# Kernel optimization log

Measured on AMD Instinct MI355X. Metric: run time of the kernel, lower is better.

Reference implementation:

```python
import jax, jax.numpy as jnp
import numpy as np

EPS = 1e-6

def elu_feature_map(x):
    return jax.nn.elu(x) + 1.0

def setup_inputs() -> dict:
    key = jax.random.key(0)
    kq, kk, kv = jax.random.split(key, 3)
    B, N, L, S, H, D, M = 4, 8, 1024, 1024, 8, 64, 64
    queries = jax.random.normal(kq, (B, N, L, H, D), dtype=jnp.float32)
    keys = jax.random.normal(kk, (B, N, S, H, D), dtype=jnp.float32)
    values = jax.random.normal(kv, (B, N, S, H, M), dtype=jnp.float32)
    key_mask = jnp.ones((B, S), dtype=jnp.float32)  # key_lengths.float_matrix (all valid)
    return {"queries": queries, "keys": keys, "values": values, "key_mask": key_mask}

def reference(queries, keys, values, key_mask):
    # Q: [B,N,L,H,D], K: [B,N,S,H,D], V: [B,N,S,H,M], key_mask: [B,S]
    Q = elu_feature_map(queries)
    K = elu_feature_map(keys) * key_mask[:, None, :, None, None]
    # KV state: [B,N,H,M,D]
    KV = jnp.einsum('bnshd,bnshm->bnhmd', K, values)
    # normalizer: [B,N,L,H]
    Z = 1.0 / (jnp.einsum('bnlhd,bnhd->bnlh', Q, K.sum(axis=2)) + EPS)
    # output: [B,N,L,H,M]
    V = jnp.einsum('bnlhd,bnhmd,bnlh->bnlhm', Q, KV, Z)
    return V
```

## Files before the change

kernel.cpp:

```cpp
#include <hip/hip_runtime.h>
#include <hip/hip_bf16.h>


constexpr int Bc = 4, Nc = 8, Hc = 8;
constexpr int Lc = 1024, Sc = 1024, Dc = 64, Mc = 64;
constexpr int HD = Hc * Dc;
constexpr int GROUPS = Bc * Nc * Hc;
constexpr int SPLITS = 4;
constexpr int SROWS = Sc / SPLITS;
constexpr int LSPLITS = 4;
constexpr int LROWS = Lc / LSPLITS;
constexpr int PARTIAL = Dc * Mc + Dc;
constexpr int NTS = SROWS / 32;
constexpr int NTL = LROWS / 64;
constexpr int PADS = 36;
constexpr int PADD = 68;
constexpr float EPSF = 1e-6f;

typedef __attribute__((ext_vector_type(8))) __bf16 bf16x8;
typedef __attribute__((ext_vector_type(4))) float f32x4;

__device__ __forceinline__ float elup1(float x) {
    return x > 0.0f ? x + 1.0f : __expf(x);
}
__device__ __forceinline__ unsigned short f2bf(float f) {
    unsigned u = __builtin_bit_cast(unsigned, f);
    u += 0x7fffu + ((u >> 16) & 1u);
    return (unsigned short)(u >> 16);
}
__device__ __forceinline__ unsigned packbf(float lo, float hi) {
    return (unsigned)f2bf(lo) | ((unsigned)f2bf(hi) << 16);
}

__global__ void __launch_bounds__(256, 4)
la_kv_mfma(const float* __restrict__ Kg, const float* __restrict__ Vg,
           const float* __restrict__ Mg, float* __restrict__ ws)
{
    __shared__ unsigned short kt[Dc][PADS];
    __shared__ unsigned short vt[Mc][PADS];
    __shared__ float ksred[16][64];

    const int t    = threadIdx.x;
    const int tx   = t & 15;
    const int tyq  = t >> 4;
    const int lane = t & 63;
    const int w    = t >> 6;
    const int g    = blockIdx.y;
    const int sp   = blockIdx.x;
    const int h    = g & 7;
    const int bn   = g >> 3;
    const int b    = g >> 6;

    const size_t rowbase = (size_t)bn * Sc * HD + (size_t)h * Dc;
    const size_t mbase   = (size_t)b * Sc;
    const int    sbase   = sp * SROWS;

    float4 kr0, kr1, vr0, vr1;
    float  mr0, mr1;
    float  ksp[4] = {0.f, 0.f, 0.f, 0.f};

    auto loadA = [&](int it) {
        const int s0 = sbase + it * 32 + 2 * tyq;
        const size_t off = rowbase + (size_t)s0 * HD + 4 * tx;
        kr0 = *reinterpret_cast<const float4*>(Kg + off);
        kr1 = *reinterpret_cast<const float4*>(Kg + off + HD);
        vr0 = *reinterpret_cast<const float4*>(Vg + off);
        vr1 = *reinterpret_cast<const float4*>(Vg + off + HD);
        mr0 = Mg[mbase + s0];
        mr1 = Mg[mbase + s0 + 1];
    };
    auto storeA = [&]() {
        const float k0[4] = {kr0.x, kr0.y, kr0.z, kr0.w};
        const float k1[4] = {kr1.x, kr1.y, kr1.z, kr1.w};
        const float v0[4] = {vr0.x, vr0.y, vr0.z, vr0.w};
        const float v1[4] = {vr1.x, vr1.y, vr1.z, vr1.w};
        #pragma unroll
        for (int i = 0; i < 4; ++i) {
            const float a0 = elup1(k0[i]) * mr0;
            const float a1 = elup1(k1[i]) * mr1;
            ksp[i] += a0 + a1;
            *reinterpret_cast<unsigned*>(&kt[4 * tx + i][2 * tyq]) = packbf(a0, a1);
            *reinterpret_cast<unsigned*>(&vt[4 * tx + i][2 * tyq]) = packbf(v0[i], v1[i]);
        }
    };

    f32x4 acc[4];
    #pragma unroll
    for (int ms = 0; ms < 4; ++ms) acc[ms] = (f32x4){0.f, 0.f, 0.f, 0.f};

    const int fcol = 8 * (lane >> 4);
    const int frow = lane & 15;

    loadA(0);
    storeA();
    __syncthreads();
    for (int it = 0; it < NTS; ++it) {
        if (it + 1 < NTS) loadA(it + 1);
        union { bf16x8 v; uint2 u[2]; } fa;
        {
            const uint2* p = reinterpret_cast<const uint2*>(&kt[16 * w + frow][fcol]);
            fa.u[0] = p[0]; fa.u[1] = p[1];
        }
        #pragma unroll
        for (int ms = 0; ms < 4; ++ms) {
            union { bf16x8 v; uint2 u[2]; } fb;
            const uint2* p = reinterpret_cast<const uint2*>(&vt[16 * ms + frow][fcol]);
            fb.u[0] = p[0]; fb.u[1] = p[1];
            acc[ms] = __builtin_amdgcn_mfma_f32_16x16x32_bf16(fa.v, fb.v, acc[ms], 0, 0, 0);
        }
        __syncthreads();
        if (it + 1 < NTS) storeA();
        __syncthreads();
    }

    float* outp = ws + (size_t)(g * SPLITS + sp) * PARTIAL;
    #pragma unroll
    for (int ms = 0; ms < 4; ++ms)
        #pragma unroll
        for (int r = 0; r < 4; ++r)
            outp[(16 * w + 4 * (lane >> 4) + r) * Mc + 16 * ms + frow] = acc[ms][r];

    #pragma unroll
    for (int i = 0; i < 4; ++i) ksred[tyq][4 * tx + i] = ksp[i];
    __syncthreads();
    if (t < 64) {
        float s = 0.f;
        #pragma unroll
        for (int j = 0; j < 16; ++j) s += ksred[j][t];
        outp[Dc * Mc + t] = s;
    }
}

__global__ void __launch_bounds__(256, 4)
la_out_mfma(const float* __restrict__ Qg, const float* __restrict__ ws,
            float* __restrict__ Og)
{
    __shared__ unsigned short kvm[Mc][PADD];
    __shared__ unsigned short ksb[64];
    __shared__ unsigned short qb[64][PADD];

    const int t    = threadIdx.x;
    const int tx   = t & 15;
    const int tyq  = t >> 4;
    const int lane = t & 63;
    const int w    = t >> 6;
    const int g    = blockIdx.y;
    const int ls   = blockIdx.x;
    const int h    = g & 7;
    const int bn   = g >> 3;

    const size_t rowbase = (size_t)bn * Lc * HD + (size_t)h * Dc;
    const float* pw = ws + (size_t)g * SPLITS * PARTIAL;
    const int lbase = ls * LROWS;

    float4 qr[4];
    auto loadB = [&](int it) {
        const int l0 = lbase + it * 64 + 4 * tyq;
        #pragma unroll
        for (int j = 0; j < 4; ++j)
            qr[j] = *reinterpret_cast<const float4*>(Qg + rowbase + (size_t)(l0 + j) * HD + 4 * tx);
    };
    auto storeB = [&]() {
        #pragma unroll
        for (int j = 0; j < 4; ++j) {
            const int r = 4 * tyq + j;
            const float q[4] = {qr[j].x, qr[j].y, qr[j].z, qr[j].w};
            uint2 pk;
            pk.x = packbf(elup1(q[0]), elup1(q[1]));
            pk.y = packbf(elup1(q[2]), elup1(q[3]));
            *reinterpret_cast<uint2*>(&qb[r][4 * tx]) = pk;
        }
    };

    loadB(0);
    #pragma unroll
    for (int e = 0; e < 16; ++e) {
        const int idx = t + 256 * e;
        const float s = pw[idx] + pw[PARTIAL + idx] + pw[2 * PARTIAL + idx] + pw[3 * PARTIAL + idx];
        kvm[idx & 63][idx >> 6] = f2bf(s);
    }
    if (t < 64) {
        const float s = pw[Dc * Mc + t] + pw[PARTIAL + Dc * Mc + t]
                      + pw[2 * PARTIAL + Dc * Mc + t] + pw[3 * PARTIAL + Dc * Mc + t];
        ksb[t] = f2bf(s);
    }
    storeB();
    __syncthreads();

    const int fcol = 8 * (lane >> 4);
    const int frow = lane & 15;

    bf16x8 bkv[2][4], bks[2];
    #pragma unroll
    for (int ks = 0; ks < 2; ++ks) {
        #pragma unroll
        for (int ms = 0; ms < 4; ++ms) {
            union { bf16x8 v; uint2 u[2]; } f;
            const uint2* p = reinterpret_cast<const uint2*>(&kvm[16 * ms + frow][32 * ks + fcol]);
            f.u[0] = p[0]; f.u[1] = p[1];
            bkv[ks][ms] = f.v;
        }
        union { bf16x8 v; uint2 u[2]; } fz;
        const uint2* p = reinterpret_cast<const uint2*>(&ksb[32 * ks + fcol]);
        fz.u[0] = p[0]; fz.u[1] = p[1];
        bks[ks] = fz.v;
    }

    const size_t obase = (size_t)bn * Lc * HD + (size_t)h * Mc;
    for (int it = 0; it < NTL; ++it) {
        if (it + 1 < NTL) loadB(it + 1);
        union { bf16x8 v; uint2 u[2]; } fa0, fa1;
        {
            const uint2* p0 = reinterpret_cast<const uint2*>(&qb[16 * w + frow][fcol]);
            fa0.u[0] = p0[0]; fa0.u[1] = p0[1];
            const uint2* p1 = reinterpret_cast<const uint2*>(&qb[16 * w + frow][32 + fcol]);
            fa1.u[0] = p1[0]; fa1.u[1] = p1[1];
        }
        f32x4 acc[4], accz;
        #pragma unroll
        for (int ms = 0; ms < 4; ++ms) acc[ms] = (f32x4){0.f, 0.f, 0.f, 0.f};
        accz = (f32x4){0.f, 0.f, 0.f, 0.f};
        #pragma unroll
        for (int ms = 0; ms < 4; ++ms) {
            acc[ms] = __builtin_amdgcn_mfma_f32_16x16x32_bf16(fa0.v, bkv[0][ms], acc[ms], 0, 0, 0);
            acc[ms] = __builtin_amdgcn_mfma_f32_16x16x32_bf16(fa1.v, bkv[1][ms], acc[ms], 0, 0, 0);
        }
        accz = __builtin_amdgcn_mfma_f32_16x16x32_bf16(fa0.v, bks[0], accz, 0, 0, 0);
        accz = __builtin_amdgcn_mfma_f32_16x16x32_bf16(fa1.v, bks[1], accz, 0, 0, 0);

        const int lt = lbase + it * 64 + 16 * w + 4 * (lane >> 4);
        #pragma unroll
        for (int r = 0; r < 4; ++r) {
            const float z = 1.0f / (accz[r] + EPSF);
            const size_t ro = obase + (size_t)(lt + r) * HD + frow;
            #pragma unroll
            for (int ms = 0; ms < 4; ++ms)
                Og[ro + 16 * ms] = acc[ms][r] * z;
        }
        __syncthreads();
        if (it + 1 < NTL) storeB();
        __syncthreads();
    }
}

__global__ void __launch_bounds__(256, 1)
la_fused_kernel(const float* __restrict__ Qg, const float* __restrict__ Kg,
                const float* __restrict__ Vg, const float* __restrict__ Mg,
                float* __restrict__ Og)
{
    __shared__ float lk[32][Dc];
    __shared__ float lv[32][Mc];
    __shared__ float kvt[Dc][Mc];
    __shared__ float ksm[Dc];
    __shared__ float qt[Dc][64];

    const int t  = threadIdx.x;
    const int tx = t & 15;
    const int ty = t >> 4;
    const int g  = blockIdx.x;
    const int h  = g & 7;
    const int bn = g >> 3;
    const int b  = g >> 6;

    const size_t rowbase = (size_t)bn * Sc * HD + (size_t)h * Dc;
    const size_t mbase   = (size_t)b * Sc;

    const int d0 = tx * 4, m0 = ty * 4, c4 = tx * 4, r0 = ty;

    float acc[4][4] = {{0.f,0.f,0.f,0.f},{0.f,0.f,0.f,0.f},{0.f,0.f,0.f,0.f},{0.f,0.f,0.f,0.f}};
    float ks[4] = {0.f, 0.f, 0.f, 0.f};
    float4 kr[2], vr[2];
    float  mr[2];

    auto loadA = [&](int it) {
        const int s0 = it * 32;
        #pragma unroll
        for (int k = 0; k < 2; ++k) {
            const int r = r0 + 16 * k;
            const size_t off = rowbase + (size_t)(s0 + r) * HD + c4;
            kr[k] = *reinterpret_cast<const float4*>(Kg + off);
            vr[k] = *reinterpret_cast<const float4*>(Vg + off);
            mr[k] = Mg[mbase + s0 + r];
        }
    };
    auto storeA = [&]() {
        #pragma unroll
        for (int k = 0; k < 2; ++k) {
            const int r = r0 + 16 * k;
            float4 kk;
            kk.x = elup1(kr[k].x) * mr[k];
            kk.y = elup1(kr[k].y) * mr[k];
            kk.z = elup1(kr[k].z) * mr[k];
            kk.w = elup1(kr[k].w) * mr[k];
            *reinterpret_cast<float4*>(&lk[r][c4]) = kk;
            *reinterpret_cast<float4*>(&lv[r][c4]) = vr[k];
        }
    };

    loadA(0);
    storeA();
    __syncthreads();
    for (int it = 0; it < Sc / 32; ++it) {
        if (it + 1 < Sc / 32) loadA(it + 1);
        #pragma unroll 8
        for (int r = 0; r < 32; ++r) {
            const float4 k4 = *reinterpret_cast<const float4*>(&lk[r][d0]);
            const float4 v4 = *reinterpret_cast<const float4*>(&lv[r][m0]);
            const float kk[4] = {k4.x, k4.y, k4.z, k4.w};
            const float vv[4] = {v4.x, v4.y, v4.z, v4.w};
            ks[0] += kk[0]; ks[1] += kk[1]; ks[2] += kk[2]; ks[3] += kk[3];
            #pragma unroll
            for (int i = 0; i < 4; ++i)
                #pragma unroll
                for (int j = 0; j < 4; ++j)
                    acc[i][j] += kk[i] * vv[j];
        }
        __syncthreads();
        if (it + 1 < Sc / 32) storeA();
        __syncthreads();
    }

    #pragma unroll
    for (int i = 0; i < 4; ++i) {
        float4 w;
        w.x = acc[i][0]; w.y = acc[i][1]; w.z = acc[i][2]; w.w = acc[i][3];
        *reinterpret_cast<float4*>(&kvt[d0 + i][m0]) = w;
    }
    if (ty == 0) {
        #pragma unroll
        for (int i = 0; i < 4; ++i) ksm[d0 + i] = ks[i];
    }
    __syncthreads();

    float4 qr[4];
    auto loadB = [&](int it) {
        const int l0 = it * 64;
        #pragma unroll
        for (int k = 0; k < 4; ++k) {
            const int r = r0 + 16 * k;
            const size_t off = rowbase + (size_t)(l0 + r) * HD + c4;
            qr[k] = *reinterpret_cast<const float4*>(Qg + off);
        }
    };
    const int swzw = (tx & 7) << 2;
    auto storeB = [&]() {
        #pragma unroll
        for (int k = 0; k < 4; ++k) {
            const int r = r0 + 16 * k;
            const int lidx = r ^ swzw;
            qt[c4 + 0][lidx] = elup1(qr[k].x);
            qt[c4 + 1][lidx] = elup1(qr[k].y);
            qt[c4 + 2][lidx] = elup1(qr[k].z);
            qt[c4 + 3][lidx] = elup1(qr[k].w);
        }
    };

    loadB(0);
    storeB();
    __syncthreads();
    for (int it = 0; it < Lc / 64; ++it) {
        if (it + 1 < Lc / 64) loadB(it + 1);
        float accB[4][4] = {{0.f,0.f,0.f,0.f},{0.f,0.f,0.f,0.f},{0.f,0.f,0.f,0.f},{0.f,0.f,0.f,0.f}};
        float za[4] = {0.f, 0.f, 0.f, 0.f};
        #pragma unroll 8
        for (int d = 0; d < Dc; ++d) {
            const int swz = ((d >> 2) & 7) << 2;
            const float4 q4  = *reinterpret_cast<const float4*>(&qt[d][(4 * ty) ^ swz]);
            const float4 kv4 = *reinterpret_cast<const float4*>(&kvt[d][4 * tx]);
            const float kd = ksm[d];
            const float qq[4] = {q4.x, q4.y, q4.z, q4.w};
            const float kv[4] = {kv4.x, kv4.y, kv4.z, kv4.w};
            #pragma unroll
            for (int i = 0; i < 4; ++i) {
                za[i] += qq[i] * kd;
                #pragma unroll
                for (int j = 0; j < 4; ++j)
                    accB[i][j] += qq[i] * kv[j];
            }
        }
        const int l0 = it * 64;
        const size_t obase = (size_t)bn * Lc * HD + (size_t)h * Mc;
        #pragma unroll
        for (int i = 0; i < 4; ++i) {
            const int l = l0 + 4 * ty + i;
            const float z = 1.0f / (za[i] + EPSF);
            float4 o;
            o.x = accB[i][0] * z; o.y = accB[i][1] * z;
            o.z = accB[i][2] * z; o.w = accB[i][3] * z;
            *reinterpret_cast<float4*>(Og + obase + (size_t)l * HD + 4 * tx) = o;
        }
        __syncthreads();
        if (it + 1 < Lc / 64) storeB();
        __syncthreads();
    }
}

extern "C" void kernel_launch(void* const* d_in, const int* in_sizes, int n_in,
                              void* d_out, int out_size, void* d_ws, size_t ws_size,
                              hipStream_t stream) {
    const float* Qg = (const float*)d_in[0];
    const float* Kg = (const float*)d_in[1];
    const float* Vg = (const float*)d_in[2];
    const float* Mg = (const float*)d_in[3];
    float* Og = (float*)d_out;

    const size_t need = (size_t)GROUPS * SPLITS * PARTIAL * sizeof(float);
    if (ws_size >= need) {
        float* ws = (float*)d_ws;
        hipLaunchKernelGGL(la_kv_mfma, dim3(SPLITS, GROUPS), dim3(256), 0, stream,
                           Kg, Vg, Mg, ws);
        hipLaunchKernelGGL(la_out_mfma, dim3(LSPLITS, GROUPS), dim3(256), 0, stream,
                           Qg, ws, Og);
    } else {
        hipLaunchKernelGGL(la_fused_kernel, dim3(GROUPS), dim3(256), 0, stream,
                           Qg, Kg, Vg, Mg, Og);
    }
}
```

Measured before the change: 67.93 us.

## Use split-bf16 three-term MFMA for accuracy and double-buffer KV staging

Both MFMA kernels now split every fp32 operand into high and low bf16 parts and run three MFMAs per product (hi*hi, hi*lo, lo*hi). This approximates fp32 accuracy instead of plain bf16. The KV kernel also double-buffers its shared-memory staging with two register load sets, which drops one barrier per tile. The key sum moves from a shared-memory reduction to an MFMA against a ones fragment. This roughly triples matrix work and doubles LDS traffic and footprint, so the change mainly buys precision at some speed cost.

New measurement: 74.64 us. 1.1x slower.

```diff
diff --git a/kernel.cpp b/kernel.cpp
--- a/kernel.cpp
+++ b/kernel.cpp
@@ -6,12 +6,9 @@
 constexpr int Lc = 1024, Sc = 1024, Dc = 64, Mc = 64;
 constexpr int HD = Hc * Dc;
 constexpr int GROUPS = Bc * Nc * Hc;
-constexpr int SPLITS = 4;
-constexpr int SROWS = Sc / SPLITS;
 constexpr int LSPLITS = 4;
 constexpr int LROWS = Lc / LSPLITS;
 constexpr int PARTIAL = Dc * Mc + Dc;
-constexpr int NTS = SROWS / 32;
 constexpr int NTL = LROWS / 64;
 constexpr int PADS = 36;
 constexpr int PADD = 68;
@@ -28,17 +25,35 @@
     u += 0x7fffu + ((u >> 16) & 1u);
     return (unsigned short)(u >> 16);
 }
-__device__ __forceinline__ unsigned packbf(float lo, float hi) {
-    return (unsigned)f2bf(lo) | ((unsigned)f2bf(hi) << 16);
-}
-
+__device__ __forceinline__ float bf2f(unsigned short h) {
+    return __builtin_bit_cast(float, (unsigned)h << 16);
+}
+__device__ __forceinline__ void splitbf(float x, unsigned short& h, unsigned short& l) {
+    h = f2bf(x);
+    l = f2bf(x - bf2f(h));
+}
+__device__ __forceinline__ unsigned pack2(unsigned short lo, unsigned short hi) {
+    return (unsigned)lo | ((unsigned)hi << 16);
+}
+__device__ __forceinline__ bf16x8 ones_frag() {
+    union { bf16x8 v; unsigned short s[8]; } u;
+    #pragma unroll
+    for (int i = 0; i < 8; ++i) u.s[i] = 0x3F80;
+    return u.v;
+}
+
+template<int NSPL>
 __global__ void __launch_bounds__(256, 4)
 la_kv_mfma(const float* __restrict__ Kg, const float* __restrict__ Vg,
            const float* __restrict__ Mg, float* __restrict__ ws)
 {
-    __shared__ unsigned short kt[Dc][PADS];
-    __shared__ unsigned short vt[Mc][PADS];
-    __shared__ float ksred[16][64];
+    constexpr int SR = Sc / NSPL;
+    constexpr int NT = SR / 32;
+
+    __shared__ unsigned short kth[2][Dc][PADS];
+    __shared__ unsigned short ktl[2][Dc][PADS];
+    __shared__ unsigned short vth[2][Dc][PADS];
+    __shared__ unsigned short vtl[2][Dc][PADS];
 
     const int t    = threadIdx.x;
     const int tx   = t & 15;
@@ -53,91 +68,127 @@
 
     const size_t rowbase = (size_t)bn * Sc * HD + (size_t)h * Dc;
     const size_t mbase   = (size_t)b * Sc;
-    const int    sbase   = sp * SROWS;
-
-    float4 kr0, kr1, vr0, vr1;
-    float  mr0, mr1;
-    float  ksp[4] = {0.f, 0.f, 0.f, 0.f};
-
-    auto loadA = [&](int it) {
+    const int    sbase   = sp * SR;
+
+    float4 kA0, kA1, vA0, vA1; float2 mA;
+    float4 kB0, kB1, vB0, vB1; float2 mB;
+
+    auto loadA_A = [&](int it) {
         const int s0 = sbase + it * 32 + 2 * tyq;
         const size_t off = rowbase + (size_t)s0 * HD + 4 * tx;
-        kr0 = *reinterpret_cast<const float4*>(Kg + off);
-        kr1 = *reinterpret_cast<const float4*>(Kg + off + HD);
-        vr0 = *reinterpret_cast<const float4*>(Vg + off);
-        vr1 = *reinterpret_cast<const float4*>(Vg + off + HD);
-        mr0 = Mg[mbase + s0];
-        mr1 = Mg[mbase + s0 + 1];
-    };
-    auto storeA = [&]() {
-        const float k0[4] = {kr0.x, kr0.y, kr0.z, kr0.w};
-        const float k1[4] = {kr1.x, kr1.y, kr1.z, kr1.w};
-        const float v0[4] = {vr0.x, vr0.y, vr0.z, vr0.w};
-        const float v1[4] = {vr1.x, vr1.y, vr1.z, vr1.w};
+        kA0 = *reinterpret_cast<const float4*>(Kg + off);
+        kA1 = *reinterpret_cast<const float4*>(Kg + off + HD);
+        vA0 = *reinterpret_cast<const float4*>(Vg + off);
+        vA1 = *reinterpret_cast<const float4*>(Vg + off + HD);
+        mA  = *reinterpret_cast<const float2*>(Mg + mbase + s0);
+    };
+    auto loadA_B = [&](int it) {
+        const int s0 = sbase + it * 32 + 2 * tyq;
+        const size_t off = rowbase + (size_t)s0 * HD + 4 * tx;
+        kB0 = *reinterpret_cast<const float4*>(Kg + off);
+        kB1 = *reinterpret_cast<const float4*>(Kg + off + HD);
+        vB0 = *reinterpret_cast<const float4*>(Vg + off);
+        vB1 = *reinterpret_cast<const float4*>(Vg + off + HD);
+        mB  = *reinterpret_cast<const float2*>(Mg + mbase + s0);
+    };
+    auto stage = [&](int buf, const float4& K0, const float4& K1,
+                     const float4& V0, const float4& V1, const float2& M2) {
+        const float k0[4] = {K0.x, K0.y, K0.z, K0.w};
+        const float k1[4] = {K1.x, K1.y, K1.z, K1.w};
+        const float v0[4] = {V0.x, V0.y, V0.z, V0.w};
+        const float v1[4] = {V1.x, V1.y, V1.z, V1.w};
         #pragma unroll
         for (int i = 0; i < 4; ++i) {
-            const float a0 = elup1(k0[i]) * mr0;
-            const float a1 = elup1(k1[i]) * mr1;
-            ksp[i] += a0 + a1;
-            *reinterpret_cast<unsigned*>(&kt[4 * tx + i][2 * tyq]) = packbf(a0, a1);
-            *reinterpret_cast<unsigned*>(&vt[4 * tx + i][2 * tyq]) = packbf(v0[i], v1[i]);
-        }
-    };
-
-    f32x4 acc[4];
+            const float a0 = elup1(k0[i]) * M2.x;
+            const float a1 = elup1(k1[i]) * M2.y;
+            unsigned short h0, l0, h1, l1;
+            splitbf(a0, h0, l0);
+            splitbf(a1, h1, l1);
+            *reinterpret_cast<unsigned*>(&kth[buf][4 * tx + i][2 * tyq]) = pack2(h0, h1);
+            *reinterpret_cast<unsigned*>(&ktl[buf][4 * tx + i][2 * tyq]) = pack2(l0, l1);
+            unsigned short vh0, vl0, vh1, vl1;
+            splitbf(v0[i], vh0, vl0);
+            splitbf(v1[i], vh1, vl1);
+            *reinterpret_cast<unsigned*>(&vth[buf][4 * tx + i][2 * tyq]) = pack2(vh0, vh1);
+            *reinterpret_cast<unsigned*>(&vtl[buf][4 * tx + i][2 * tyq]) = pack2(vl0, vl1);
+        }
+    };
+
+    f32x4 acc[4], aks;
     #pragma unroll
     for (int ms = 0; ms < 4; ++ms) acc[ms] = (f32x4){0.f, 0.f, 0.f, 0.f};
+    aks = (f32x4){0.f, 0.f, 0.f, 0.f};
+    const bf16x8 ones = ones_frag();
 
     const int fcol = 8 * (lane >> 4);
     const int frow = lane & 15;
 
-    loadA(0);
-    storeA();
+    auto compute = [&](int buf) {
+        union { bf16x8 v; uint2 u[2]; } fah, fal;
+        {
+            const uint2* ph = reinterpret_cast<const uint2*>(&kth[buf][16 * w + frow][fcol]);
+            fah.u[0] = ph[0]; fah.u[1] = ph[1];
+            const uint2* pl = reinterpret_cast<const uint2*>(&ktl[buf][16 * w + frow][fcol]);
+            fal.u[0] = pl[0]; fal.u[1] = pl[1];
+        }
+        aks = __builtin_amdgcn_mfma_f32_16x16x32_bf16(fah.v, ones, aks, 0, 0, 0);
+        aks = __builtin_amdgcn_mfma_f32_16x16x32_bf16(fal.v, ones, aks, 0, 0, 0);
+        #pragma unroll
+        for (int ms = 0; ms < 4; ++ms) {
+            union { bf16x8 v; uint2 u[2]; } fbh, fbl;
+            const uint2* ph = reinterpret_cast<const uint2*>(&vth[buf][16 * ms + frow][fcol]);
+            fbh.u[0] = ph[0]; fbh.u[1] = ph[1];
+            const uint2* pl = reinterpret_cast<const uint2*>(&vtl[buf][16 * ms + frow][fcol]);
+            fbl.u[0] = pl[0]; fbl.u[1] = pl[1];
+            acc[ms] = __builtin_amdgcn_mfma_f32_16x16x32_bf16(fah.v, fbh.v, acc[ms], 0, 0, 0);
+            acc[ms] = __builtin_amdgcn_mfma_f32_16x16x32_bf16(fah.v, fbl.v, acc[ms], 0, 0, 0);
+            acc[ms] = __builtin_amdgcn_mfma_f32_16x16x32_bf16(fal.v, fbh.v, acc[ms], 0, 0, 0);
+        }
+    };
+
+    loadA_A(0);
+    loadA_B(1);
+    stage(0, kA0, kA1, vA0, vA1, mA);
+    loadA_A(2);
     __syncthreads();
-    for (int it = 0; it < NTS; ++it) {
-        if (it + 1 < NTS) loadA(it + 1);
-        union { bf16x8 v; uint2 u[2]; } fa;
-        {
-            const uint2* p = reinterpret_cast<const uint2*>(&kt[16 * w + frow][fcol]);
-            fa.u[0] = p[0]; fa.u[1] = p[1];
-        }
-        #pragma unroll
-        for (int ms = 0; ms < 4; ++ms) {
-            union { bf16x8 v; uint2 u[2]; } fb;
-            const uint2* p = reinterpret_cast<const uint2*>(&vt[16 * ms + frow][fcol]);
-            fb.u[0] = p[0]; fb.u[1] = p[1];
-            acc[ms] = __builtin_amdgcn_mfma_f32_16x16x32_bf16(fa.v, fb.v, acc[ms], 0, 0, 0);
-        }
-        __syncthreads();
-        if (it + 1 < NTS) storeA();
-        __syncthreads();
-    }
-
-    float* outp = ws + (size_t)(g * SPLITS + sp) * PARTIAL;
+
+    for (int it = 0; it < NT; it += 2) {
+        compute(0);
+        stage(1, kB0, kB1, vB0, vB1, mB);
+        if (it + 3 < NT) loadA_B(it + 3);
+        __syncthreads();
+
+        compute(1);
+        if (it + 2 < NT) stage(0, kA0, kA1, vA0, vA1, mA);
+        if (it + 4 < NT) loadA_A(it + 4);
+        __syncthreads();
+    }
+
+    float* outp = ws + (size_t)(g * NSPL + sp) * PARTIAL;
     #pragma unroll
     for (int ms = 0; ms < 4; ++ms)
         #pragma unroll
         for (int r = 0; r < 4; ++r)
             outp[(16 * w + 4 * (lane >> 4) + r) * Mc + 16 * ms + frow] = acc[ms][r];
 
-    #pragma unroll
-    for (int i = 0; i < 4; ++i) ksred[tyq][4 * tx + i] = ksp[i];
-    __syncthreads();
-    if (t < 64) {
-        float s = 0.f;
-        #pragma unroll
-        for (int j = 0; j < 16; ++j) s += ksred[j][t];
-        outp[Dc * Mc + t] = s;
-    }
-}
-
+    if (frow == 0) {
+        #pragma unroll
+        for (int r = 0; r < 4; ++r)
+            outp[Dc * Mc + 16 * w + 4 * (lane >> 4) + r] = aks[r];
+    }
+}
+
+template<int NSPL>
 __global__ void __launch_bounds__(256, 4)
 la_out_mfma(const float* __restrict__ Qg, const float* __restrict__ ws,
             float* __restrict__ Og)
 {
-    __shared__ unsigned short kvm[Mc][PADD];
-    __shared__ unsigned short ksb[64];
-    __shared__ unsigned short qb[64][PADD];
+    __shared__ unsigned short kvh[Mc][PADD];
+    __shared__ unsigned short kvl[Mc][PADD];
+    __shared__ unsigned short ksh[64];
+    __shared__ unsigned short ksl[64];
+    __shared__ unsigned short qhh[64][PADD];
+    __shared__ unsigned short qll[64][PADD];
 
     const int t    = threadIdx.x;
     const int tx   = t & 15;
@@ -150,7 +201,7 @@
     const int bn   = g >> 3;
 
     const size_t rowbase = (size_t)bn * Lc * HD + (size_t)h * Dc;
-    const float* pw = ws + (size_t)g * SPLITS * PARTIAL;
+    const float* pw = ws + (size_t)g * NSPL * PARTIAL;
     const int lbase = ls * LROWS;
 
     float4 qr[4];
@@ -165,10 +216,16 @@
         for (int j = 0; j < 4; ++j) {
             const int r = 4 * tyq + j;
             const float q[4] = {qr[j].x, qr[j].y, qr[j].z, qr[j].w};
-            uint2 pk;
-            pk.x = packbf(elup1(q[0]), elup1(q[1]));
-            pk.y = packbf(elup1(q[2]), elup1(q[3]));
-            *reinterpret_cast<uint2*>(&qb[r][4 * tx]) = pk;
+            unsigned short h0, l0, h1, l1, h2, l2, h3, l3;
+            splitbf(elup1(q[0]), h0, l0);
+            splitbf(elup1(q[1]), h1, l1);
+            splitbf(elup1(q[2]), h2, l2);
+            splitbf(elup1(q[3]), h3, l3);
+            uint2 ph, pl;
+            ph.x = pack2(h0, h1); ph.y = pack2(h2, h3);
+            pl.x = pack2(l0, l1); pl.y = pack2(l2, l3);
+            *reinterpret_cast<uint2*>(&qhh[r][4 * tx]) = ph;
+            *reinterpret_cast<uint2*>(&qll[r][4 * tx]) = pl;
         }
     };
 
@@ -176,57 +233,69 @@
     #pragma unroll
     for (int e = 0; e < 16; ++e) {
         const int idx = t + 256 * e;
-        const float s = pw[idx] + pw[PARTIAL + idx] + pw[2 * PARTIAL + idx] + pw[3 * PARTIAL + idx];
-        kvm[idx & 63][idx >> 6] = f2bf(s);
+        float s = 0.f;
+        #pragma unroll
+        for (int sp = 0; sp < NSPL; ++sp) s += pw[sp * PARTIAL + idx];
+        unsigned short hh, ll;
+        splitbf(s, hh, ll);
+        kvh[idx & 63][idx >> 6] = hh;
+        kvl[idx & 63][idx >> 6] = ll;
     }
     if (t < 64) {
-        const float s = pw[Dc * Mc + t] + pw[PARTIAL + Dc * Mc + t]
-                      + pw[2 * PARTIAL + Dc * Mc + t] + pw[3 * PARTIAL + Dc * Mc + t];
-        ksb[t] = f2bf(s);
+        float s = 0.f;
+        #pragma unroll
+        for (int sp = 0; sp < NSPL; ++sp) s += pw[sp * PARTIAL + Dc * Mc + t];
+        unsigned short hh, ll;
+        splitbf(s, hh, ll);
+        ksh[t] = hh;
+        ksl[t] = ll;
     }
     storeB();
     __syncthreads();
 
     const int fcol = 8 * (lane >> 4);
     const int frow = lane & 15;
-
-    bf16x8 bkv[2][4], bks[2];
-    #pragma unroll
-    for (int ks = 0; ks < 2; ++ks) {
-        #pragma unroll
-        for (int ms = 0; ms < 4; ++ms) {
-            union { bf16x8 v; uint2 u[2]; } f;
-            const uint2* p = reinterpret_cast<const uint2*>(&kvm[16 * ms + frow][32 * ks + fcol]);
-            f.u[0] = p[0]; f.u[1] = p[1];
-            bkv[ks][ms] = f.v;
-        }
-        union { bf16x8 v; uint2 u[2]; } fz;
-        const uint2* p = reinterpret_cast<const uint2*>(&ksb[32 * ks + fcol]);
-        fz.u[0] = p[0]; fz.u[1] = p[1];
-        bks[ks] = fz.v;
-    }
-
     const size_t obase = (size_t)bn * Lc * HD + (size_t)h * Mc;
+
     for (int it = 0; it < NTL; ++it) {
         if (it + 1 < NTL) loadB(it + 1);
-        union { bf16x8 v; uint2 u[2]; } fa0, fa1;
+        union { bf16x8 v; uint2 u[2]; } fah0, fal0, fah1, fal1;
         {
-            const uint2* p0 = reinterpret_cast<const uint2*>(&qb[16 * w + frow][fcol]);
-            fa0.u[0] = p0[0]; fa0.u[1] = p0[1];
-            const uint2* p1 = reinterpret_cast<const uint2*>(&qb[16 * w + frow][32 + fcol]);
-            fa1.u[0] = p1[0]; fa1.u[1] = p1[1];
+            const uint2* p;
+            p = reinterpret_cast<const uint2*>(&qhh[16 * w + frow][fcol]);      fah0.u[0] = p[0]; fah0.u[1] = p[1];
+            p = reinterpret_cast<const uint2*>(&qll[16 * w + frow][fcol]);      fal0.u[0] = p[0]; fal0.u[1] = p[1];
+            p = reinterpret_cast<const uint2*>(&qhh[16 * w + frow][32 + fcol]); fah1.u[0] = p[0]; fah1.u[1] = p[1];
+            p = reinterpret_cast<const uint2*>(&qll[16 * w + frow][32 + fcol]); fal1.u[0] = p[0]; fal1.u[1] = p[1];
         }
         f32x4 acc[4], accz;
         #pragma unroll
         for (int ms = 0; ms < 4; ++ms) acc[ms] = (f32x4){0.f, 0.f, 0.f, 0.f};
         accz = (f32x4){0.f, 0.f, 0.f, 0.f};
-        #pragma unroll
-        for (int ms = 0; ms < 4; ++ms) {
-            acc[ms] = __builtin_amdgcn_mfma_f32_16x16x32_bf16(fa0.v, bkv[0][ms], acc[ms], 0, 0, 0);
-            acc[ms] = __builtin_amdgcn_mfma_f32_16x16x32_bf16(fa1.v, bkv[1][ms], acc[ms], 0, 0, 0);
-        }
-        accz = __builtin_amdgcn_mfma_f32_16x16x32_bf16(fa0.v, bks[0], accz, 0, 0, 0);
-        accz = __builtin_amdgcn_mfma_f32_16x16x32_bf16(fa1.v, bks[1], accz, 0, 0, 0);
+
+        #pragma unroll
+        for (int ks = 0; ks < 2; ++ks) {
+            const bf16x8 fh = ks ? fah1.v : fah0.v;
+            const bf16x8 fl = ks ? fal1.v : fal0.v;
+            #pragma unroll
+            for (int ms = 0; ms < 4; ++ms) {
+                union { bf16x8 v; uint2 u[2]; } fbh, fbl;
+                const uint2* ph = reinterpret_cast<const uint2*>(&kvh[16 * ms + frow][32 * ks + fcol]);
+                fbh.u[0] = ph[0]; fbh.u[1] = ph[1];
+                const uint2* pl = reinterpret_cast<const uint2*>(&kvl[16 * ms + frow][32 * ks + fcol]);
+                fbl.u[0] = pl[0]; fbl.u[1] = pl[1];
+                acc[ms] = __builtin_amdgcn_mfma_f32_16x16x32_bf16(fh, fbh.v, acc[ms], 0, 0, 0);
+                acc[ms] = __builtin_amdgcn_mfma_f32_16x16x32_bf16(fh, fbl.v, acc[ms], 0, 0, 0);
+                acc[ms] = __builtin_amdgcn_mfma_f32_16x16x32_bf16(fl, fbh.v, acc[ms], 0, 0, 0);
+            }
+            union { bf16x8 v; uint2 u[2]; } fzh, fzl;
+            const uint2* ph = reinterpret_cast<const uint2*>(&ksh[32 * ks + fcol]);
+            fzh.u[0] = ph[0]; fzh.u[1] = ph[1];
+            const uint2* pl = reinterpret_cast<const uint2*>(&ksl[32 * ks + fcol]);
+            fzl.u[0] = pl[0]; fzl.u[1] = pl[1];
+            accz = __builtin_amdgcn_mfma_f32_16x16x32_bf16(fh, fzh.v, accz, 0, 0, 0);
+            accz = __builtin_amdgcn_mfma_f32_16x16x32_bf16(fh, fzl.v, accz, 0, 0, 0);
+            accz = __builtin_amdgcn_mfma_f32_16x16x32_bf16(fl, fzh.v, accz, 0, 0, 0);
+        }
 
         const int lt = lbase + it * 64 + 16 * w + 4 * (lane >> 4);
         #pragma unroll
@@ -404,12 +473,12 @@
     const float* Mg = (const float*)d_in[3];
     float* Og = (float*)d_out;
 
-    const size_t need = (size_t)GROUPS * SPLITS * PARTIAL * sizeof(float);
-    if (ws_size >= need) {
+    const size_t need4 = (size_t)GROUPS * 4 * PARTIAL * sizeof(float);
+    if (ws_size >= need4) {
         float* ws = (float*)d_ws;
-        hipLaunchKernelGGL(la_kv_mfma, dim3(SPLITS, GROUPS), dim3(256), 0, stream,
+        hipLaunchKernelGGL((la_kv_mfma<4>), dim3(4, GROUPS), dim3(256), 0, stream,
                            Kg, Vg, Mg, ws);
-        hipLaunchKernelGGL(la_out_mfma, dim3(LSPLITS, GROUPS), dim3(256), 0, stream,
+        hipLaunchKernelGGL((la_out_mfma<4>), dim3(LSPLITS, GROUPS), dim3(256), 0, stream,
                            Qg, ws, Og);
     } else {
         hipLaunchKernelGGL(la_fused_kernel, dim3(GROUPS), dim3(256), 0, stream,
```
